# Optimization experiments

Hardware: AMD Instinct MI355X
Metric: run time of the kernel (lower is better)

The kernel has to match this reference:

```python
import jax, jax.numpy as jnp
import numpy as np

B, T, H = 2, 512, 256


def setup_inputs() -> dict:
    key = jax.random.key(0)
    k1, k2, k3, k4, k5 = jax.random.split(key, 5)
    scale = 1.0 / np.sqrt(H)
    Q = jax.random.normal(k1, (B, T, H), dtype=jnp.float32)
    K = jax.random.normal(k2, (B, T, H), dtype=jnp.float32)
    # torch nn.Linear weights: y = x @ W.T, W shape [out, in]
    Wq = jax.random.normal(k3, (H, H), dtype=jnp.float32) * scale
    Wk = jax.random.normal(k4, (H, H), dtype=jnp.float32) * scale
    v = jax.random.normal(k5, (H,), dtype=jnp.float32) * scale  # Linear(H,1) weight
    return {"Q": Q, "K": K, "Wq": Wq, "Wk": Wk, "v": v}


def reference(Q, K, Wq, Wk, v):
    # Project queries and keys: [B,T,H]
    Qp = jnp.einsum("bth,oh->bto", Q, Wq)
    Kp = jnp.einsum("bsh,oh->bso", K, Wk)
    # Additive (Bahdanau) scores: tanh over broadcast sum -> [B,T,T,H], then v-proj -> [B,T,T]
    e = jnp.tanh(Qp[:, :, None, :] + Kp[:, None, :, :])
    scores = jnp.einsum("btsh,h->bts", e, v)
    # Causal mask: query t may only attend to keys s <= t
    mask = jnp.tril(jnp.ones((T, T), dtype=bool))
    scores = jnp.where(mask[None, :, :], scores, jnp.float32(-1e9))
    alpha = jax.nn.softmax(scores, axis=-1)
    # Weighted sum of (raw) K values: [B,T,H]
    ctx = jnp.einsum("bts,bsh->bth", alpha, K)
    return ctx, alpha
```

## Files before the change

### kernel.cpp

```cpp
#include <hip/hip_runtime.h>

#define BB 2
#define TT 512
#define HH 256
#define NBT (BB * TT)

#define C2LOG2E 2.8853900817779268f

__global__ __launch_bounds__(256) void proj_kernel(
    const float* __restrict__ Q, const float* __restrict__ K,
    const float* __restrict__ Wq, const float* __restrict__ Wk,
    float* __restrict__ Eq, float* __restrict__ EkT)
{
    const int ROWS = 8;
    int grp = blockIdx.x;
    const int nQ = NBT / ROWS;
    bool isK = (grp >= nQ);
    int bt0 = (isK ? grp - nQ : grp) * ROWS;
    const float* X = isK ? K : Q;
    const float* W = isK ? Wk : Wq;

    int o = threadIdx.x;
    const float4* w4p = reinterpret_cast<const float4*>(W + o * HH);
    const float4* x4p = reinterpret_cast<const float4*>(X + bt0 * HH);

    float acc[ROWS] = {0.f, 0.f, 0.f, 0.f, 0.f, 0.f, 0.f, 0.f};
#pragma unroll 2
    for (int h4 = 0; h4 < HH / 4; ++h4) {
        float4 w4 = w4p[h4];
#pragma unroll
        for (int r = 0; r < ROWS; ++r) {
            float4 x4 = x4p[r * (HH / 4) + h4];
            acc[r] += x4.x * w4.x + x4.y * w4.y + x4.z * w4.z + x4.w * w4.w;
        }
    }
    if (!isK) {
#pragma unroll
        for (int r = 0; r < ROWS; ++r)
            Eq[(bt0 + r) * HH + o] = __builtin_amdgcn_exp2f(acc[r] * C2LOG2E);
    } else {
        int h4 = o >> 2, c = o & 3;
#pragma unroll
        for (int r = 0; r < ROWS; ++r)
            EkT[(h4 * NBT + bt0 + r) * 4 + c] = __builtin_amdgcn_exp2f(acc[r] * C2LOG2E);
    }
}

__global__ __launch_bounds__(512, 8) void attn_kernel(
    const float* __restrict__ Eq, const float* __restrict__ EkT,
    const float* __restrict__ Kraw, const float* __restrict__ v,
    float* __restrict__ ctx, float* __restrict__ alpha)
{
    int bt = blockIdx.x;
    int b = bt / TT;
    int idx = bt % TT;
    int t = (idx < 256) ? idx : 767 - idx;
    int btr = b * TT + t;
    int tid = threadIdx.x;

    __shared__ float eq_sh[HH];
    __shared__ float v2_sh[HH];
    __shared__ float al_sh[TT];
    __shared__ float red[8];
    __shared__ float4 cred[8][64];

    if (tid < HH) {
        eq_sh[tid] = Eq[btr * HH + tid];
        v2_sh[tid] = -2.0f * v[tid];
    }
    __syncthreads();

    const float4* q4p = reinterpret_cast<const float4*>(eq_sh);
    const float4* v4p = reinterpret_cast<const float4*>(v2_sh);

    float sc = -3.0e38f;
    if (tid <= t) {
        const float4* ek = reinterpret_cast<const float4*>(EkT) + (b * TT + tid);
        float a = 0.f;
#pragma unroll 4
        for (int h4 = 0; h4 < HH / 4; ++h4) {
            float4 e4 = ek[h4 * NBT];
            float4 q4 = q4p[h4];
            float4 vv = v4p[h4];
            float r0 = __builtin_amdgcn_rcpf(__builtin_fmaf(q4.x, e4.x, 1.0f));
            float r1 = __builtin_amdgcn_rcpf(__builtin_fmaf(q4.y, e4.y, 1.0f));
            float r2 = __builtin_amdgcn_rcpf(__builtin_fmaf(q4.z, e4.z, 1.0f));
            float r3 = __builtin_amdgcn_rcpf(__builtin_fmaf(q4.w, e4.w, 1.0f));
            a = __builtin_fmaf(vv.x, r0, a);
            a = __builtin_fmaf(vv.y, r1, a);
            a = __builtin_fmaf(vv.z, r2, a);
            a = __builtin_fmaf(vv.w, r3, a);
        }
        sc = a;
    }

    float m = sc;
#pragma unroll
    for (int off = 32; off > 0; off >>= 1)
        m = fmaxf(m, __shfl_xor(m, off));
    int wid = tid >> 6;
    if ((tid & 63) == 0) red[wid] = m;
    __syncthreads();
    m = fmaxf(fmaxf(fmaxf(red[0], red[1]), fmaxf(red[2], red[3])),
              fmaxf(fmaxf(red[4], red[5]), fmaxf(red[6], red[7])));

    const float LOG2E = 1.4426950408889634f;
    float e = (tid <= t) ? __builtin_amdgcn_exp2f((sc - m) * LOG2E) : 0.f;
    float ssum = e;
#pragma unroll
    for (int off = 32; off > 0; off >>= 1)
        ssum += __shfl_xor(ssum, off);
    __syncthreads();
    if ((tid & 63) == 0) red[wid] = ssum;
    __syncthreads();
    float denom = (red[0] + red[1]) + (red[2] + red[3])
                + (red[4] + red[5]) + (red[6] + red[7]);
    float a0 = e * __builtin_amdgcn_rcpf(denom);

    al_sh[tid] = a0;
    alpha[btr * TT + tid] = a0;
    __syncthreads();

    int hc = tid & 63;
    int sg = tid >> 6;
    const float4* kb4 = reinterpret_cast<const float4*>(Kraw + b * TT * HH) + hc;
    float4 acc4 = {0.f, 0.f, 0.f, 0.f};
#pragma unroll 2
    for (int s = sg; s <= t; s += 8) {
        float4 k4 = kb4[s * 64];
        float  al = al_sh[s];
        acc4.x = __builtin_fmaf(al, k4.x, acc4.x);
        acc4.y = __builtin_fmaf(al, k4.y, acc4.y);
        acc4.z = __builtin_fmaf(al, k4.z, acc4.z);
        acc4.w = __builtin_fmaf(al, k4.w, acc4.w);
    }
    cred[sg][hc] = acc4;
    __syncthreads();
    if (sg == 0) {
        float4 out = {0.f, 0.f, 0.f, 0.f};
#pragma unroll
        for (int g = 0; g < 8; ++g) {
            float4 c = cred[g][hc];
            out.x += c.x; out.y += c.y; out.z += c.z; out.w += c.w;
        }
        reinterpret_cast<float4*>(ctx + btr * HH)[hc] = out;
    }
}

extern "C" void kernel_launch(void* const* d_in, const int* in_sizes, int n_in,
                              void* d_out, int out_size, void* d_ws, size_t ws_size,
                              hipStream_t stream) {
    const float* Q  = (const float*)d_in[0];
    const float* K  = (const float*)d_in[1];
    const float* Wq = (const float*)d_in[2];
    const float* Wk = (const float*)d_in[3];
    const float* v  = (const float*)d_in[4];

    float* ctx   = (float*)d_out;
    float* alpha = (float*)d_out + BB * TT * HH;

    float* Eq  = (float*)d_ws;
    float* EkT = Eq + BB * TT * HH;

    proj_kernel<<<2 * NBT / 8, 256, 0, stream>>>(Q, K, Wq, Wk, Eq, EkT);
    attn_kernel<<<NBT, 512, 0, stream>>>(Eq, EkT, K, v, ctx, alpha);
}
```

Baseline: 38.85 us.

## Store exp(K) and raw K as bf16, transpose weights, drop softmax max pass

Adds a prep kernel that transposes Wq/Wk and converts K to bf16. The projection kernel is restructured to stage input rows in shared memory and read transposed weights with coalesced float4 loads, and it writes exp(2Kp) as bf16 in a transposed layout. The attention kernel reads bf16 keys in both the score and context loops, halving that memory traffic. It also drops the softmax max reduction and one barrier, relying on scores being bounded by the sum of |v|. Risks are bf16 precision loss in alpha and ctx, plus an extra kernel launch.

After: 57.71 us. 1.49x slower.

```diff
diff --git a/kernel.cpp b/kernel.cpp
--- a/kernel.cpp
+++ b/kernel.cpp
@@ -6,51 +6,118 @@
 #define NBT (BB * TT)
 
 #define C2LOG2E 2.8853900817779268f
-
-__global__ __launch_bounds__(256) void proj_kernel(
+#define LOG2E   1.4426950408889634f
+
+__device__ __forceinline__ unsigned short f2bf(float f) {
+    unsigned u = __float_as_uint(f);
+    unsigned r = u + 0x7fffu + ((u >> 16) & 1u);
+    return (unsigned short)(r >> 16);
+}
+__device__ __forceinline__ float bflo(unsigned u) { return __uint_as_float(u << 16); }
+__device__ __forceinline__ float bfhi(unsigned u) { return __uint_as_float(u & 0xffff0000u); }
+
+__global__ __launch_bounds__(256) void prep_kernel(
+    const float* __restrict__ K, const float* __restrict__ Wq,
+    const float* __restrict__ Wk,
+    float* __restrict__ WqT, float* __restrict__ WkT,
+    unsigned short* __restrict__ K16)
+{
+    int bid = blockIdx.x;
+    int tid = threadIdx.x;
+    if (bid < 32) {
+        const float* W = (bid < 16) ? Wq : Wk;
+        float* WT = (bid < 16) ? WqT : WkT;
+        int tile = bid & 15;
+        int o0 = (tile >> 2) * 64, h0 = (tile & 3) * 64;
+        __shared__ float t_sh[64][65];
+        int ty = tid >> 6, tx = tid & 63;
+#pragma unroll
+        for (int r = 0; r < 16; ++r) {
+            int o = r * 4 + ty;
+            t_sh[o][tx] = W[(o0 + o) * HH + h0 + tx];
+        }
+        __syncthreads();
+#pragma unroll
+        for (int r = 0; r < 16; ++r) {
+            int h = r * 4 + ty;
+            WT[(h0 + h) * HH + o0 + tx] = t_sh[tx][h];
+        }
+    } else {
+        int i = (bid - 32) * 1024 + tid * 4;
+        float4 k4 = *reinterpret_cast<const float4*>(K + i);
+        ushort4 o4;
+        o4.x = f2bf(k4.x); o4.y = f2bf(k4.y); o4.z = f2bf(k4.z); o4.w = f2bf(k4.w);
+        *reinterpret_cast<ushort4*>(K16 + i) = o4;
+    }
+}
+
+__global__ __launch_bounds__(512) void proj_kernel(
     const float* __restrict__ Q, const float* __restrict__ K,
-    const float* __restrict__ Wq, const float* __restrict__ Wk,
-    float* __restrict__ Eq, float* __restrict__ EkT)
+    const float* __restrict__ WqT, const float* __restrict__ WkT,
+    float* __restrict__ Eq, unsigned short* __restrict__ EkT16)
 {
-    const int ROWS = 8;
-    int grp = blockIdx.x;
-    const int nQ = NBT / ROWS;
-    bool isK = (grp >= nQ);
-    int bt0 = (isK ? grp - nQ : grp) * ROWS;
+    __shared__ float x_sh[8][HH];
+    __shared__ unsigned short ek_sh[8][HH];
+
+    int bid = blockIdx.x;
+    bool isK = (bid >= 128);
+    int bt0 = (isK ? bid - 128 : bid) * 8;
     const float* X = isK ? K : Q;
-    const float* W = isK ? Wk : Wq;
-
-    int o = threadIdx.x;
-    const float4* w4p = reinterpret_cast<const float4*>(W + o * HH);
-    const float4* x4p = reinterpret_cast<const float4*>(X + bt0 * HH);
-
-    float acc[ROWS] = {0.f, 0.f, 0.f, 0.f, 0.f, 0.f, 0.f, 0.f};
+    const float* WT = isK ? WkT : WqT;
+    int tid = threadIdx.x;
+    int o4 = tid & 63, sg = tid >> 6;
+
+    {
+        int r = tid >> 6, h4 = tid & 63;
+        *reinterpret_cast<float4*>(&x_sh[r][h4 * 4]) =
+            *reinterpret_cast<const float4*>(X + (bt0 + r) * HH + h4 * 4);
+    }
+    __syncthreads();
+
+    const float4* wt4 = reinterpret_cast<const float4*>(WT);
+    float4 acc = {0.f, 0.f, 0.f, 0.f};
 #pragma unroll 2
-    for (int h4 = 0; h4 < HH / 4; ++h4) {
-        float4 w4 = w4p[h4];
-#pragma unroll
-        for (int r = 0; r < ROWS; ++r) {
-            float4 x4 = x4p[r * (HH / 4) + h4];
-            acc[r] += x4.x * w4.x + x4.y * w4.y + x4.z * w4.z + x4.w * w4.w;
-        }
-    }
+    for (int h4 = 0; h4 < 64; ++h4) {
+        float4 x4 = *reinterpret_cast<const float4*>(&x_sh[sg][h4 * 4]);
+        float4 w0 = wt4[(h4 * 4 + 0) * 64 + o4];
+        float4 w1 = wt4[(h4 * 4 + 1) * 64 + o4];
+        float4 w2 = wt4[(h4 * 4 + 2) * 64 + o4];
+        float4 w3 = wt4[(h4 * 4 + 3) * 64 + o4];
+        acc.x += x4.x * w0.x + x4.y * w1.x + x4.z * w2.x + x4.w * w3.x;
+        acc.y += x4.x * w0.y + x4.y * w1.y + x4.z * w2.y + x4.w * w3.y;
+        acc.z += x4.x * w0.z + x4.y * w1.z + x4.z * w2.z + x4.w * w3.z;
+        acc.w += x4.x * w0.w + x4.y * w1.w + x4.z * w2.w + x4.w * w3.w;
+    }
+    float4 e;
+    e.x = __builtin_amdgcn_exp2f(acc.x * C2LOG2E);
+    e.y = __builtin_amdgcn_exp2f(acc.y * C2LOG2E);
+    e.z = __builtin_amdgcn_exp2f(acc.z * C2LOG2E);
+    e.w = __builtin_amdgcn_exp2f(acc.w * C2LOG2E);
+
     if (!isK) {
-#pragma unroll
-        for (int r = 0; r < ROWS; ++r)
-            Eq[(bt0 + r) * HH + o] = __builtin_amdgcn_exp2f(acc[r] * C2LOG2E);
+        *reinterpret_cast<float4*>(Eq + (bt0 + sg) * HH + o4 * 4) = e;
     } else {
-        int h4 = o >> 2, c = o & 3;
-#pragma unroll
-        for (int r = 0; r < ROWS; ++r)
-            EkT[(h4 * NBT + bt0 + r) * 4 + c] = __builtin_amdgcn_exp2f(acc[r] * C2LOG2E);
+        ushort4 u;
+        u.x = f2bf(e.x); u.y = f2bf(e.y); u.z = f2bf(e.z); u.w = f2bf(e.w);
+        *reinterpret_cast<ushort4*>(&ek_sh[sg][o4 * 4]) = u;
+        __syncthreads();
+        int s_l = tid >> 4, bt_i = (tid >> 1) & 7, half = tid & 1;
+        uint2 val = *reinterpret_cast<const uint2*>(&ek_sh[bt_i][8 * s_l + 4 * half]);
+        *reinterpret_cast<uint2*>(EkT16 + (s_l * NBT + bt0 + bt_i) * 8 + 4 * half) = val;
     }
 }
 
 __global__ __launch_bounds__(512, 8) void attn_kernel(
-    const float* __restrict__ Eq, const float* __restrict__ EkT,
-    const float* __restrict__ Kraw, const float* __restrict__ v,
+    const float* __restrict__ Eq, const unsigned short* __restrict__ EkT16,
+    const unsigned short* __restrict__ K16, const float* __restrict__ v,
     float* __restrict__ ctx, float* __restrict__ alpha)
 {
+    __shared__ float eq_sh[HH];
+    __shared__ float v2_sh[HH];
+    __shared__ float al_sh[TT];
+    __shared__ float red[8];
+    __shared__ float4 cred[8][64];
+
     int bt = blockIdx.x;
     int b = bt / TT;
     int idx = bt % TT;
@@ -58,60 +125,47 @@
     int btr = b * TT + t;
     int tid = threadIdx.x;
 
-    __shared__ float eq_sh[HH];
-    __shared__ float v2_sh[HH];
-    __shared__ float al_sh[TT];
-    __shared__ float red[8];
-    __shared__ float4 cred[8][64];
-
     if (tid < HH) {
         eq_sh[tid] = Eq[btr * HH + tid];
         v2_sh[tid] = -2.0f * v[tid];
     }
     __syncthreads();
 
-    const float4* q4p = reinterpret_cast<const float4*>(eq_sh);
-    const float4* v4p = reinterpret_cast<const float4*>(v2_sh);
-
-    float sc = -3.0e38f;
+    float sc = 0.f;
     if (tid <= t) {
-        const float4* ek = reinterpret_cast<const float4*>(EkT) + (b * TT + tid);
-        float a = 0.f;
-#pragma unroll 4
-        for (int h4 = 0; h4 < HH / 4; ++h4) {
-            float4 e4 = ek[h4 * NBT];
-            float4 q4 = q4p[h4];
-            float4 vv = v4p[h4];
-            float r0 = __builtin_amdgcn_rcpf(__builtin_fmaf(q4.x, e4.x, 1.0f));
-            float r1 = __builtin_amdgcn_rcpf(__builtin_fmaf(q4.y, e4.y, 1.0f));
-            float r2 = __builtin_amdgcn_rcpf(__builtin_fmaf(q4.z, e4.z, 1.0f));
-            float r3 = __builtin_amdgcn_rcpf(__builtin_fmaf(q4.w, e4.w, 1.0f));
-            a = __builtin_fmaf(vv.x, r0, a);
-            a = __builtin_fmaf(vv.y, r1, a);
-            a = __builtin_fmaf(vv.z, r2, a);
-            a = __builtin_fmaf(vv.w, r3, a);
-        }
-        sc = a;
-    }
-
-    float m = sc;
-#pragma unroll
-    for (int off = 32; off > 0; off >>= 1)
-        m = fmaxf(m, __shfl_xor(m, off));
-    int wid = tid >> 6;
-    if ((tid & 63) == 0) red[wid] = m;
-    __syncthreads();
-    m = fmaxf(fmaxf(fmaxf(red[0], red[1]), fmaxf(red[2], red[3])),
-              fmaxf(fmaxf(red[4], red[5]), fmaxf(red[6], red[7])));
-
-    const float LOG2E = 1.4426950408889634f;
-    float e = (tid <= t) ? __builtin_amdgcn_exp2f((sc - m) * LOG2E) : 0.f;
+        const uint4* ek = reinterpret_cast<const uint4*>(EkT16) + (b * TT + tid);
+        const float4* q4p = reinterpret_cast<const float4*>(eq_sh);
+        const float4* v4p = reinterpret_cast<const float4*>(v2_sh);
+#pragma unroll 2
+        for (int h8 = 0; h8 < 32; ++h8) {
+            uint4 kk = ek[h8 * NBT];
+            float4 qa = q4p[2 * h8], qb = q4p[2 * h8 + 1];
+            float4 va = v4p[2 * h8], vb = v4p[2 * h8 + 1];
+            float r0 = __builtin_amdgcn_rcpf(__builtin_fmaf(qa.x, bflo(kk.x), 1.f));
+            float r1 = __builtin_amdgcn_rcpf(__builtin_fmaf(qa.y, bfhi(kk.x), 1.f));
+            float r2 = __builtin_amdgcn_rcpf(__builtin_fmaf(qa.z, bflo(kk.y), 1.f));
+            float r3 = __builtin_amdgcn_rcpf(__builtin_fmaf(qa.w, bfhi(kk.y), 1.f));
+            float r4 = __builtin_amdgcn_rcpf(__builtin_fmaf(qb.x, bflo(kk.z), 1.f));
+            float r5 = __builtin_amdgcn_rcpf(__builtin_fmaf(qb.y, bfhi(kk.z), 1.f));
+            float r6 = __builtin_amdgcn_rcpf(__builtin_fmaf(qb.z, bflo(kk.w), 1.f));
+            float r7 = __builtin_amdgcn_rcpf(__builtin_fmaf(qb.w, bfhi(kk.w), 1.f));
+            sc = __builtin_fmaf(va.x, r0, sc);
+            sc = __builtin_fmaf(va.y, r1, sc);
+            sc = __builtin_fmaf(va.z, r2, sc);
+            sc = __builtin_fmaf(va.w, r3, sc);
+            sc = __builtin_fmaf(vb.x, r4, sc);
+            sc = __builtin_fmaf(vb.y, r5, sc);
+            sc = __builtin_fmaf(vb.z, r6, sc);
+            sc = __builtin_fmaf(vb.w, r7, sc);
+        }
+    }
+
+    float e = (tid <= t) ? __builtin_amdgcn_exp2f(sc * LOG2E) : 0.f;
     float ssum = e;
 #pragma unroll
     for (int off = 32; off > 0; off >>= 1)
         ssum += __shfl_xor(ssum, off);
-    __syncthreads();
-    if ((tid & 63) == 0) red[wid] = ssum;
+    if ((tid & 63) == 0) red[tid >> 6] = ssum;
     __syncthreads();
     float denom = (red[0] + red[1]) + (red[2] + red[3])
                 + (red[4] + red[5]) + (red[6] + red[7]);
@@ -121,18 +175,16 @@
     alpha[btr * TT + tid] = a0;
     __syncthreads();
 
-    int hc = tid & 63;
-    int sg = tid >> 6;
-    const float4* kb4 = reinterpret_cast<const float4*>(Kraw + b * TT * HH) + hc;
+    int hc = tid & 63, sg = tid >> 6;
+    const uint2* kb = reinterpret_cast<const uint2*>(K16 + b * TT * HH);
     float4 acc4 = {0.f, 0.f, 0.f, 0.f};
-#pragma unroll 2
     for (int s = sg; s <= t; s += 8) {
-        float4 k4 = kb4[s * 64];
-        float  al = al_sh[s];
-        acc4.x = __builtin_fmaf(al, k4.x, acc4.x);
-        acc4.y = __builtin_fmaf(al, k4.y, acc4.y);
-        acc4.z = __builtin_fmaf(al, k4.z, acc4.z);
-        acc4.w = __builtin_fmaf(al, k4.w, acc4.w);
+        uint2 kk = kb[s * 64 + hc];
+        float al = al_sh[s];
+        acc4.x = __builtin_fmaf(al, bflo(kk.x), acc4.x);
+        acc4.y = __builtin_fmaf(al, bfhi(kk.x), acc4.y);
+        acc4.z = __builtin_fmaf(al, bflo(kk.y), acc4.z);
+        acc4.w = __builtin_fmaf(al, bfhi(kk.y), acc4.w);
     }
     cred[sg][hc] = acc4;
     __syncthreads();
@@ -157,11 +209,15 @@
     const float* v  = (const float*)d_in[4];
 
     float* ctx   = (float*)d_out;
-    float* alpha = (float*)d_out + BB * TT * HH;
+    float* alpha = (float*)d_out + NBT * HH;
 
     float* Eq  = (float*)d_ws;
-    float* EkT = Eq + BB * TT * HH;
-
-    proj_kernel<<<2 * NBT / 8, 256, 0, stream>>>(Q, K, Wq, Wk, Eq, EkT);
-    attn_kernel<<<NBT, 512, 0, stream>>>(Eq, EkT, K, v, ctx, alpha);
-}
+    float* WqT = Eq + NBT * HH;
+    float* WkT = WqT + HH * HH;
+    unsigned short* K16   = (unsigned short*)(WkT + HH * HH);
+    unsigned short* EkT16 = K16 + NBT * HH;
+
+    prep_kernel<<<288, 256, 0, stream>>>(K, Wq, Wk, WqT, WkT, K16);
+    proj_kernel<<<256, 512, 0, stream>>>(Q, K, WqT, WkT, Eq, EkT16);
+    attn_kernel<<<NBT, 512, 0, stream>>>(Eq, EkT16, K16, v, ctx, alpha);
+}
```
